# Kernel tuning notes

Measured on AMD Instinct MI355X. Metric: run time of the kernel, lower is better.

Reference implementation:

```python
import jax, jax.numpy as jnp
import numpy as np

LOCATE_KERNEL_STD = 0.1  # undefined global in source; chosen as a reasonable kernel width
KERNEL_MEANS = np.array([0.0, 0.2, 0.4, 0.6, 0.8, 1.0], dtype=np.float32)  # 'setof6'


def setup_inputs() -> dict:
    key = jax.random.key(0)
    k1, k2 = jax.random.split(key)
    values = jax.random.normal(k1, (16384, 2048), dtype=jnp.float32)
    # nn.Parameter(torch.rand(6) - 0.5)
    kernel_weights = jax.random.uniform(k2, (6,), dtype=jnp.float32) - 0.5
    return {"values": values, "kernel_weights": kernel_weights}


def reference(values, kernel_weights):
    bs, L_in = values.shape
    L = L_in - 2  # ret has inp.size(1) - 2 positions
    means = jnp.asarray(KERNEL_MEANS, dtype=values.dtype)  # [K]
    std = jnp.asarray(LOCATE_KERNEL_STD, dtype=values.dtype)
    # positions pos/ln for pos in range(L)
    pos = jnp.arange(L, dtype=values.dtype) / L  # [L]
    # Gaussian pdf = exp(Normal(mean, std).log_prob(pos)), vectorized over kernels x positions
    z = (pos[None, :] - means[:, None]) / std  # [K, L]
    log_norm = jnp.log(std * jnp.sqrt(2.0 * jnp.pi))
    pdf = jnp.exp(-0.5 * z * z - log_norm)  # [K, L]
    # weights = 0.25 * tanh(param); weighted sum over kernels (same for every batch row)
    w = 0.25 * jnp.tanh(kernel_weights)  # [K]
    row = w @ pdf  # [L]
    out = jnp.tanh(jnp.broadcast_to(row[None, :], (bs, L)))  # [bs, L]
    return out
```

## Files before the change

kernel.cpp:

```cpp
#include <hip/hip_runtime.h>
#include <hip/hip_bf16.h>
#include <math.h>

#define LOG_NORM_NEG 1.3836465597f

__global__ void locate_row_kernel(const float* __restrict__ kw,
                                  float* __restrict__ row, int L) {
    int c = blockIdx.x * blockDim.x + threadIdx.x;
    if (c >= L) return;
    const float means[6] = {0.0f, 0.2f, 0.4f, 0.6f, 0.8f, 1.0f};
    float pos = (float)c / (float)L;
    float s = 0.0f;
#pragma unroll
    for (int k = 0; k < 6; ++k) {
        float w = 0.25f * tanhf(kw[k]);
        float z = (pos - means[k]) * 10.0f;
        float pdf = expf(fmaf(-0.5f * z, z, LOG_NORM_NEG));
        s = fmaf(w, pdf, s);
    }
    row[c] = tanhf(s);
}

__global__ void locate_broadcast_kernel(const float* __restrict__ row,
                                        float4* __restrict__ out,
                                        unsigned int L, unsigned int total4) {
    unsigned int i = blockIdx.x * blockDim.x + threadIdx.x;
    if (i >= total4) return;
    unsigned int base = i * 4u;
    unsigned int c = base % L;
    float4 v;
    v.x = row[c]; ++c; if (c == L) c = 0;
    v.y = row[c]; ++c; if (c == L) c = 0;
    v.z = row[c]; ++c; if (c == L) c = 0;
    v.w = row[c];
    out[i] = v;
}

__global__ void locate_fused_kernel(const float* __restrict__ kw,
                                    float* __restrict__ out,
                                    unsigned int L, unsigned int total) {
    unsigned int i = blockIdx.x * blockDim.x + threadIdx.x;
    if (i >= total) return;
    const float means[6] = {0.0f, 0.2f, 0.4f, 0.6f, 0.8f, 1.0f};
    unsigned int c = i % L;
    float pos = (float)c / (float)L;
    float s = 0.0f;
#pragma unroll
    for (int k = 0; k < 6; ++k) {
        float w = 0.25f * tanhf(kw[k]);
        float z = (pos - means[k]) * 10.0f;
        float pdf = expf(fmaf(-0.5f * z, z, LOG_NORM_NEG));
        s = fmaf(w, pdf, s);
    }
    out[i] = tanhf(s);
}

extern "C" void kernel_launch(void* const* d_in, const int* in_sizes, int n_in,
                              void* d_out, int out_size, void* d_ws, size_t ws_size,
                              hipStream_t stream) {
    const float* kw = (const float*)d_in[1];
    float* out = (float*)d_out;

    long long n_values = in_sizes[0];
    long long bs = (n_values - (long long)out_size) / 2;
    int L = (int)((long long)out_size / bs);

    unsigned int total = (unsigned int)out_size;
    if (ws_size >= (size_t)L * sizeof(float)) {
        float* row = (float*)d_ws;
        {
            int threads = 256;
            int blocks = (L + threads - 1) / threads;
            locate_row_kernel<<<blocks, threads, 0, stream>>>(kw, row, L);
        }
        {
            unsigned int total4 = total / 4u;
            int threads = 256;
            int blocks = (int)((total4 + threads - 1) / threads);
            locate_broadcast_kernel<<<blocks, threads, 0, stream>>>(
                row, (float4*)out, (unsigned int)L, total4);
        }
    } else {
        int threads = 256;
        int blocks = (int)((total + threads - 1) / threads);
        locate_fused_kernel<<<blocks, threads, 0, stream>>>(
            kw, out, (unsigned int)L, total);
    }
}
```

Before: 212.4 us.

## Preload row pairs in registers and stream rows with nontemporal stores

Replaces the per-element broadcast kernel with one where each block loads two output rows' worth of the row vector into registers once, then writes many row pairs with nontemporal vector stores. This is meant to remove the repeated modulo indexing and row reads per output element and to keep the large write stream from polluting the cache. The fallback path now reads the precomputed row and drops the workspace-size check, so it assumes the workspace is always big enough.

```diff
diff --git a/kernel.cpp b/kernel.cpp
--- a/kernel.cpp
+++ b/kernel.cpp
@@ -3,6 +3,8 @@
 #include <math.h>
 
 #define LOG_NORM_NEG 1.3836465597f
+
+typedef float f32x4 __attribute__((ext_vector_type(4)));
 
 __global__ void locate_row_kernel(const float* __restrict__ kw,
                                   float* __restrict__ row, int L) {
@@ -21,38 +23,48 @@
     row[c] = tanhf(s);
 }
 
-__global__ void locate_broadcast_kernel(const float* __restrict__ row,
-                                        float4* __restrict__ out,
-                                        unsigned int L, unsigned int total4) {
-    unsigned int i = blockIdx.x * blockDim.x + threadIdx.x;
-    if (i >= total4) return;
-    unsigned int base = i * 4u;
-    unsigned int c = base % L;
-    float4 v;
-    v.x = row[c]; ++c; if (c == L) c = 0;
-    v.y = row[c]; ++c; if (c == L) c = 0;
-    v.z = row[c]; ++c; if (c == L) c = 0;
-    v.w = row[c];
-    out[i] = v;
+#define NV 4
+
+__global__ __launch_bounds__(256) void locate_broadcast2(
+    const float* __restrict__ row, f32x4* __restrict__ out4,
+    int L, int pairs, int ppb) {
+    const int nvec = (2 * L) / 4;
+    const int tid  = threadIdx.x;
+
+    f32x4 v[NV];
+#pragma unroll
+    for (int i = 0; i < NV; ++i) {
+        int j = tid + i * 256;
+        if (j < nvec) {
+            int c = (4 * j) % L;
+            f32x4 t;
+            t.x = row[c]; ++c; if (c == L) c = 0;
+            t.y = row[c]; ++c; if (c == L) c = 0;
+            t.z = row[c]; ++c; if (c == L) c = 0;
+            t.w = row[c];
+            v[i] = t;
+        }
+    }
+
+    const int p0 = blockIdx.x * ppb;
+    for (int k = 0; k < ppb; ++k) {
+        int p = p0 + k;
+        if (p >= pairs) return;
+        f32x4* dst = out4 + (size_t)p * (size_t)nvec;
+#pragma unroll
+        for (int i = 0; i < NV; ++i) {
+            int j = tid + i * 256;
+            if (j < nvec) __builtin_nontemporal_store(v[i], dst + j);
+        }
+    }
 }
 
-__global__ void locate_fused_kernel(const float* __restrict__ kw,
+__global__ void locate_fused_kernel(const float* __restrict__ row,
                                     float* __restrict__ out,
                                     unsigned int L, unsigned int total) {
     unsigned int i = blockIdx.x * blockDim.x + threadIdx.x;
     if (i >= total) return;
-    const float means[6] = {0.0f, 0.2f, 0.4f, 0.6f, 0.8f, 1.0f};
-    unsigned int c = i % L;
-    float pos = (float)c / (float)L;
-    float s = 0.0f;
-#pragma unroll
-    for (int k = 0; k < 6; ++k) {
-        float w = 0.25f * tanhf(kw[k]);
-        float z = (pos - means[k]) * 10.0f;
-        float pdf = expf(fmaf(-0.5f * z, z, LOG_NORM_NEG));
-        s = fmaf(w, pdf, s);
-    }
-    out[i] = tanhf(s);
+    out[i] = row[i % L];
 }
 
 extern "C" void kernel_launch(void* const* d_in, const int* in_sizes, int n_in,
@@ -65,25 +77,25 @@
     long long bs = (n_values - (long long)out_size) / 2;
     int L = (int)((long long)out_size / bs);
 
-    unsigned int total = (unsigned int)out_size;
-    if (ws_size >= (size_t)L * sizeof(float)) {
-        float* row = (float*)d_ws;
-        {
-            int threads = 256;
-            int blocks = (L + threads - 1) / threads;
-            locate_row_kernel<<<blocks, threads, 0, stream>>>(kw, row, L);
-        }
-        {
-            unsigned int total4 = total / 4u;
-            int threads = 256;
-            int blocks = (int)((total4 + threads - 1) / threads);
-            locate_broadcast_kernel<<<blocks, threads, 0, stream>>>(
-                row, (float4*)out, (unsigned int)L, total4);
-        }
+    float* row = (float*)d_ws;
+    {
+        int threads = 256;
+        int blocks = (L + threads - 1) / threads;
+        locate_row_kernel<<<blocks, threads, 0, stream>>>(kw, row, L);
+    }
+
+    bool pair_ok = (bs % 2 == 0) && ((2 * L) % 4 == 0) && ((2 * L) / 4 <= NV * 256);
+    if (pair_ok) {
+        int pairs = (int)(bs / 2);
+        int ppb = (pairs + 1023) / 1024;
+        int blocks = (pairs + ppb - 1) / ppb;
+        locate_broadcast2<<<blocks, 256, 0, stream>>>(
+            row, (f32x4*)out, L, pairs, ppb);
     } else {
+        unsigned int total = (unsigned int)out_size;
         int threads = 256;
         int blocks = (int)((total + threads - 1) / threads);
         locate_fused_kernel<<<blocks, threads, 0, stream>>>(
-            kw, out, (unsigned int)L, total);
+            row, out, (unsigned int)L, total);
     }
 }
```

Result: no change. 210.2 us (-1.1%).
